# Kernel optimization log

Measured on AMD Instinct MI355X. Metric: run time of the kernel, lower is better.

Reference implementation:

```python
import jax, jax.numpy as jnp
import numpy as np

B, T, E, UNITS, VOCAB, NCLS = 128, 512, 256, 256, 50257, 2

def setup_inputs() -> dict:
    key = jax.random.key(0)
    ks = jax.random.split(key, 7)
    s = 0.05
    return {
        "sentence": jax.random.randint(ks[0], (B, T), 0, VOCAB, dtype=jnp.int32),
        "emb_table": jax.random.normal(ks[1], (VOCAB, E), jnp.float32) * s,
        "W": jax.random.normal(ks[2], (1, UNITS, E), jnp.float32) * s,
        "U": jax.random.normal(ks[3], (1, UNITS, UNITS), jnp.float32) * s,
        "W1": jax.random.normal(ks[4], (UNITS, 32), jnp.float32) * s,
        "b1": jnp.zeros((32,), jnp.float32),
        "W2": jax.random.normal(ks[5], (32, NCLS), jnp.float32) * s,
        "b2": jnp.zeros((NCLS,), jnp.float32),
    }

def reference(sentence, emb_table, W, U, W1, b1, W2, b2):
    # Embedding lookup: [B, T, E]
    emb = emb_table[sentence]
    # Precompute input projection for all timesteps in one batched GEMM:
    # x @ W[0].T for every t -> [T, B, units]
    xW = jnp.einsum('bte,ue->tbu', emb, W[0])
    Ut = U[0].T  # [units, units]

    def step(h, xw_t):
        h_new = jnp.tanh(xw_t + h @ Ut)
        return h_new, None

    h0 = jnp.zeros((sentence.shape[0], W.shape[1]), emb.dtype)
    h_final, _ = jax.lax.scan(step, h0, xW)

    # Classification head (dropout is identity at inference)
    hidden = jax.nn.relu(h_final @ W1 + b1)
    logits = hidden @ W2 + b2
    return jax.nn.softmax(logits, axis=-1)
```

## Files before the change

### kernel.cpp

```cpp
#include <hip/hip_runtime.h>
#include <hip/hip_bf16.h>
#include <stdint.h>

#define TT 512
#define NB 128
#define EM 256
#define UN 256

typedef float floatx4 __attribute__((ext_vector_type(4)));
typedef int v8i __attribute__((ext_vector_type(8)));

#define SCALE_Q 0x7B7B7B7BU
#define SCALE_A 0x7D7D7D7DU

#define BAR() asm volatile("s_waitcnt lgkmcnt(0)\n\ts_barrier" ::: "memory")

__device__ inline unsigned short f2bf(float f) {
    union { float f; uint32_t u; } v; v.f = f;
    uint32_t r = v.u + 0x7fffu + ((v.u >> 16) & 1u);
    return (unsigned short)(r >> 16);
}
__device__ inline unsigned char f2fp8(float f) {
    int pk = __builtin_amdgcn_cvt_pk_fp8_f32(f, f, 0, false);
    return (unsigned char)(pk & 0xff);
}
__device__ inline float fp8dec(uint32_t word, int sel) {
#if defined(__has_builtin)
#if __has_builtin(__builtin_amdgcn_cvt_f32_fp8)
    return __builtin_amdgcn_cvt_f32_fp8(word >> (8 * sel), 0);
#else
    unsigned char b = (word >> (8 * sel)) & 0xff;
    int s = b >> 7, e = (b >> 3) & 15, m = b & 7;
    float v = e ? ldexpf((float)(8 + m), e - 10) : ldexpf((float)m, -9);
    return s ? -v : v;
#endif
#else
    unsigned char b = (word >> (8 * sel)) & 0xff;
    int s = b >> 7, e = (b >> 3) & 15, m = b & 7;
    float v = e ? ldexpf((float)(8 + m), e - 10) : ldexpf((float)m, -9);
    return s ? -v : v;
#endif
}

__global__ void k_pack(const float* __restrict__ W, const float* __restrict__ U,
                       unsigned char* __restrict__ wfrag8, unsigned char* __restrict__ ufrag8) {
    int bid = blockIdx.x;
    const float* src = (bid < 32) ? W : U;
    unsigned char* dstbase = (bid < 32) ? wfrag8 : ufrag8;
    int idx = (bid & 31) * 256 + threadIdx.x;
    int jg   = idx & 3;
    int lane = (idx >> 2) & 63;
    int tile = idx >> 8;
    int nt = tile & 15, kh = tile >> 4;
    int u  = nt * 16 + (lane & 15);
    int k0 = kh * 128 + (lane >> 4) * 32 + jg * 8;
    unsigned char* dst = dstbase + ((size_t)tile * 64 + lane) * 32 + jg * 8;
    #pragma unroll
    for (int j = 0; j < 8; j++) dst[j] = f2fp8(16.f * src[u * EM + k0 + j]);
}

__global__ __launch_bounds__(256, 2) void k_gemm(
    const int* __restrict__ sent, const float* __restrict__ emb,
    const unsigned char* __restrict__ wfrag8, unsigned char* __restrict__ xw8)
{
    __shared__ unsigned char gt[64][272];
    int w    = threadIdx.x >> 6;
    int lane = threadIdx.x & 63;
    int m  = lane & 15;
    int kg = lane >> 4;
    int row = blockIdx.x * 64 + w * 16 + m;
    int tok = sent[row];
    const float* arow = emb + (size_t)tok * EM;

    union { uint32_t d[8]; v8i v; } A[2];
    #pragma unroll
    for (int kh = 0; kh < 2; kh++) {
        const float* p = arow + kh * 128 + kg * 32;
        #pragma unroll
        for (int d = 0; d < 8; d++) {
            float4 f = *(const float4*)(p + 4 * d);
            int pk = __builtin_amdgcn_cvt_pk_fp8_f32(16.f * f.x, 16.f * f.y, 0, false);
            pk     = __builtin_amdgcn_cvt_pk_fp8_f32(16.f * f.z, 16.f * f.w, pk, true);
            A[kh].d[d] = (uint32_t)pk;
        }
    }

    const floatx4 zero4 = {0.f, 0.f, 0.f, 0.f};
    floatx4 acc[16];
    #pragma unroll
    for (int nt = 0; nt < 16; nt++) {
        union { uint4 u4[2]; v8i v; } B0, B1;
        const uint4* p0 = (const uint4*)(wfrag8 + ((size_t)(0 * 16 + nt) * 64 + lane) * 32);
        const uint4* p1 = (const uint4*)(wfrag8 + ((size_t)(1 * 16 + nt) * 64 + lane) * 32);
        B0.u4[0] = p0[0]; B0.u4[1] = p0[1];
        B1.u4[0] = p1[0]; B1.u4[1] = p1[1];
        floatx4 a = __builtin_amdgcn_mfma_scale_f32_16x16x128_f8f6f4(
                        A[0].v, B0.v, zero4, 0, 0, 0, SCALE_Q, 0, SCALE_Q);
        a = __builtin_amdgcn_mfma_scale_f32_16x16x128_f8f6f4(
                        A[1].v, B1.v, a, 0, 0, 0, SCALE_Q, 0, SCALE_Q);
        acc[nt] = a;
    }

    int rloc = w * 16 + kg * 4;
    #pragma unroll
    for (int nt = 0; nt < 16; nt++) {
        #pragma unroll
        for (int r = 0; r < 4; r++) {
            gt[rloc + r][nt * 16 + m] = f2fp8(16.f * acc[nt][r]);
        }
    }
    __syncthreads();

    int rowbase = blockIdx.x * 64;
    #pragma unroll
    for (int r2 = 0; r2 < 16; r2++) {
        int rr = w * 16 + r2;
        uint32_t v = *(const uint32_t*)&gt[rr][lane * 4];
        *(uint32_t*)(xw8 + (size_t)(rowbase + rr) * UN + lane * 4) = v;
    }
}

__global__ __launch_bounds__(256, 1) void k_rnn(
    const unsigned char* __restrict__ ufrag8, const unsigned char* __restrict__ xw8,
    const float* __restrict__ W1, const float* __restrict__ b1,
    const float* __restrict__ W2, const float* __restrict__ b2,
    float* __restrict__ out)
{
    __shared__ __align__(16) unsigned char hb8[2][256];
    __shared__ __align__(16) unsigned char xstage[64 * 256];
    __shared__ float hid[32];
    const int t    = threadIdx.x;
    const int lane = t & 63;
    const int w    = t >> 6;
    const int kg   = lane >> 4;
    const int b    = blockIdx.x;

    v8i ufr8[4][2];
    #pragma unroll
    for (int q = 0; q < 4; q++) {
        #pragma unroll
        for (int kh = 0; kh < 2; kh++) {
            const uint4* p = (const uint4*)(ufrag8 + ((size_t)(kh * 16 + 4 * w + q) * 64 + lane) * 32);
            union { uint4 u4[2]; v8i v; } cvt;
            cvt.u4[0] = p[0]; cvt.u4[1] = p[1];
            ufr8[q][kh] = cvt.v;
        }
    }

    const unsigned char* xwb = xw8 + (size_t)b * TT * UN;
    const int roff = t * 16;

    uint4 xr[4];
    #pragma unroll
    for (int p = 0; p < 4; p++) xr[p] = *(const uint4*)(xwb + roff + p * 4096);
    #pragma unroll
    for (int p = 0; p < 4; p++) *(uint4*)&xstage[roff + p * 4096] = xr[p];

    hb8[0][t] = 0; hb8[1][t] = 0;
    __syncthreads();

    int cur = 0;
    const float c3 = -0.33333334f, c5 = 0.13333334f, c7 = -0.05396825f, c9 = 0.02186949f;
    const floatx4 zero4 = {0.f, 0.f, 0.f, 0.f};
    const int sel = lane >> 4;

    for (int s = 0; s < TT; s++) {
        const int ls = s & 63;
        uint32_t xword = *(const uint32_t*)&xstage[ls * 256 + (t & ~3)];
        float xf = fp8dec(xword, t & 3) * 0.0625f;

        const unsigned char* hc = hb8[cur];
        union { uint4 u4[2]; v8i v; } A0, A1;
        A0.u4[0] = *(const uint4*)(hc + kg * 32);
        A0.u4[1] = *(const uint4*)(hc + kg * 32 + 16);
        A1.u4[0] = *(const uint4*)(hc + 128 + kg * 32);
        A1.u4[1] = *(const uint4*)(hc + 128 + kg * 32 + 16);

        float z[4];
        #pragma unroll
        for (int q = 0; q < 4; q++) {
            floatx4 acc = __builtin_amdgcn_mfma_scale_f32_16x16x128_f8f6f4(
                              A0.v, ufr8[q][0], zero4, 0, 0, 0, SCALE_A, 0, SCALE_Q);
            acc = __builtin_amdgcn_mfma_scale_f32_16x16x128_f8f6f4(
                              A1.v, ufr8[q][1], acc, 0, 0, 0, SCALE_A, 0, SCALE_Q);
            z[q] = acc[0];
        }

        float zz = (sel == 0) ? z[0] : (sel == 1) ? z[1] : (sel == 2) ? z[2] : z[3];
        zz += xf;

        float hn;
        if (__builtin_expect(fabsf(zz) > 0.75f, 0)) {
            float e = __expf(2.f * zz);
            hn = 1.f - 2.f * __builtin_amdgcn_rcpf(e + 1.f);
        } else {
            float x2f = zz * zz;
            float p = fmaf(x2f, c9, c7);
            p = fmaf(x2f, p, c5);
            p = fmaf(x2f, p, c3);
            hn = fmaf(zz * x2f, p, zz);
        }

        hb8[cur ^ 1][t] = f2fp8(4.f * hn);

        if (ls == 60 && s + 68 <= TT) {
            const unsigned char* cb = xwb + (size_t)(s + 4) * UN;
            #pragma unroll
            for (int p = 0; p < 4; p++) xr[p] = *(const uint4*)(cb + roff + p * 4096);
        }
        if (ls == 63 && s + 65 <= TT) {
            BAR();
            #pragma unroll
            for (int p = 0; p < 4; p++) *(uint4*)&xstage[roff + p * 4096] = xr[p];
        }
        BAR();
        cur ^= 1;
    }

    if (t < 32) {
        float a = b1[t];
        for (int k = 0; k < 256; k++) {
            uint32_t wd = *(const uint32_t*)&hb8[cur][k & ~3];
            a += 0.25f * fp8dec(wd, k & 3) * W1[k * 32 + t];
        }
        hid[t] = fmaxf(a, 0.f);
    }
    __syncthreads();
    if (t == 0) {
        float l0 = b2[0], l1 = b2[1];
        #pragma unroll
        for (int i = 0; i < 32; i++) {
            float hv = hid[i];
            l0 += hv * W2[2 * i];
            l1 += hv * W2[2 * i + 1];
        }
        float mx2 = fmaxf(l0, l1);
        float e0 = __expf(l0 - mx2), e1 = __expf(l1 - mx2);
        float inv = 1.f / (e0 + e1);
        out[2 * b]     = e0 * inv;
        out[2 * b + 1] = e1 * inv;
    }
}

extern "C" void kernel_launch(void* const* d_in, const int* in_sizes, int n_in,
                              void* d_out, int out_size, void* d_ws, size_t ws_size,
                              hipStream_t stream) {
    const int*   sent = (const int*)d_in[0];
    const float* emb  = (const float*)d_in[1];
    const float* W    = (const float*)d_in[2];
    const float* U    = (const float*)d_in[3];
    const float* W1   = (const float*)d_in[4];
    const float* b1   = (const float*)d_in[5];
    const float* W2   = (const float*)d_in[6];
    const float* b2   = (const float*)d_in[7];
    float* out = (float*)d_out;

    unsigned char* xw8    = (unsigned char*)d_ws;
    unsigned char* wfrag8 = (unsigned char*)d_ws + (size_t)NB * TT * UN;
    unsigned char* ufrag8 = wfrag8 + (size_t)UN * EM;

    k_pack<<<64, 256, 0, stream>>>(W, U, wfrag8, ufrag8);
    k_gemm<<<(NB * TT) / 64, 256, 0, stream>>>(sent, emb, wfrag8, xw8);
    k_rnn<<<NB, 256, 0, stream>>>(ufrag8, xw8, W1, b1, W2, b2, out);
}
```

Measured before the change: 302.5 us.

## Fuse input-projection GEMM into RNN kernel, computed in chunks interleaved with the recurrence

Removes the separate k_gemm kernel and its global xW buffer. Each RNN block now holds the W fragments in registers, computes the first 64 timesteps of x·Wᵀ up front, and then computes the next chunk into a double-buffered LDS array spread over the serial loop: token loads, embedding loads and the MFMA plus pack each land on different phases. The aim is to hide the projection work in idle time of the latency-bound recurrence and avoid the global round trip through the fp8 workspace. It costs more registers (W fragments plus 16 float4 prefetch) and adds work to some steps of the critical loop.

```diff
diff --git a/kernel.cpp b/kernel.cpp
--- a/kernel.cpp
+++ b/kernel.cpp
@@ -6,6 +6,7 @@
 #define NB 128
 #define EM 256
 #define UN 256
+#define XS 68
 
 typedef float floatx4 __attribute__((ext_vector_type(4)));
 typedef int v8i __attribute__((ext_vector_type(8)));
@@ -15,31 +16,12 @@
 
 #define BAR() asm volatile("s_waitcnt lgkmcnt(0)\n\ts_barrier" ::: "memory")
 
-__device__ inline unsigned short f2bf(float f) {
-    union { float f; uint32_t u; } v; v.f = f;
-    uint32_t r = v.u + 0x7fffu + ((v.u >> 16) & 1u);
-    return (unsigned short)(r >> 16);
-}
 __device__ inline unsigned char f2fp8(float f) {
     int pk = __builtin_amdgcn_cvt_pk_fp8_f32(f, f, 0, false);
     return (unsigned char)(pk & 0xff);
 }
 __device__ inline float fp8dec(uint32_t word, int sel) {
-#if defined(__has_builtin)
-#if __has_builtin(__builtin_amdgcn_cvt_f32_fp8)
     return __builtin_amdgcn_cvt_f32_fp8(word >> (8 * sel), 0);
-#else
-    unsigned char b = (word >> (8 * sel)) & 0xff;
-    int s = b >> 7, e = (b >> 3) & 15, m = b & 7;
-    float v = e ? ldexpf((float)(8 + m), e - 10) : ldexpf((float)m, -9);
-    return s ? -v : v;
-#endif
-#else
-    unsigned char b = (word >> (8 * sel)) & 0xff;
-    int s = b >> 7, e = (b >> 3) & 15, m = b & 7;
-    float v = e ? ldexpf((float)(8 + m), e - 10) : ldexpf((float)m, -9);
-    return s ? -v : v;
-#endif
 }
 
 __global__ void k_pack(const float* __restrict__ W, const float* __restrict__ U,
@@ -59,115 +41,86 @@
     for (int j = 0; j < 8; j++) dst[j] = f2fp8(16.f * src[u * EM + k0 + j]);
 }
 
-__global__ __launch_bounds__(256, 2) void k_gemm(
+__global__ __launch_bounds__(256, 1) void k_rnn(
     const int* __restrict__ sent, const float* __restrict__ emb,
-    const unsigned char* __restrict__ wfrag8, unsigned char* __restrict__ xw8)
-{
-    __shared__ unsigned char gt[64][272];
-    int w    = threadIdx.x >> 6;
-    int lane = threadIdx.x & 63;
-    int m  = lane & 15;
-    int kg = lane >> 4;
-    int row = blockIdx.x * 64 + w * 16 + m;
-    int tok = sent[row];
-    const float* arow = emb + (size_t)tok * EM;
-
-    union { uint32_t d[8]; v8i v; } A[2];
-    #pragma unroll
-    for (int kh = 0; kh < 2; kh++) {
-        const float* p = arow + kh * 128 + kg * 32;
-        #pragma unroll
-        for (int d = 0; d < 8; d++) {
-            float4 f = *(const float4*)(p + 4 * d);
-            int pk = __builtin_amdgcn_cvt_pk_fp8_f32(16.f * f.x, 16.f * f.y, 0, false);
-            pk     = __builtin_amdgcn_cvt_pk_fp8_f32(16.f * f.z, 16.f * f.w, pk, true);
-            A[kh].d[d] = (uint32_t)pk;
-        }
-    }
-
-    const floatx4 zero4 = {0.f, 0.f, 0.f, 0.f};
-    floatx4 acc[16];
-    #pragma unroll
-    for (int nt = 0; nt < 16; nt++) {
-        union { uint4 u4[2]; v8i v; } B0, B1;
-        const uint4* p0 = (const uint4*)(wfrag8 + ((size_t)(0 * 16 + nt) * 64 + lane) * 32);
-        const uint4* p1 = (const uint4*)(wfrag8 + ((size_t)(1 * 16 + nt) * 64 + lane) * 32);
-        B0.u4[0] = p0[0]; B0.u4[1] = p0[1];
-        B1.u4[0] = p1[0]; B1.u4[1] = p1[1];
-        floatx4 a = __builtin_amdgcn_mfma_scale_f32_16x16x128_f8f6f4(
-                        A[0].v, B0.v, zero4, 0, 0, 0, SCALE_Q, 0, SCALE_Q);
-        a = __builtin_amdgcn_mfma_scale_f32_16x16x128_f8f6f4(
-                        A[1].v, B1.v, a, 0, 0, 0, SCALE_Q, 0, SCALE_Q);
-        acc[nt] = a;
-    }
-
-    int rloc = w * 16 + kg * 4;
-    #pragma unroll
-    for (int nt = 0; nt < 16; nt++) {
-        #pragma unroll
-        for (int r = 0; r < 4; r++) {
-            gt[rloc + r][nt * 16 + m] = f2fp8(16.f * acc[nt][r]);
-        }
-    }
-    __syncthreads();
-
-    int rowbase = blockIdx.x * 64;
-    #pragma unroll
-    for (int r2 = 0; r2 < 16; r2++) {
-        int rr = w * 16 + r2;
-        uint32_t v = *(const uint32_t*)&gt[rr][lane * 4];
-        *(uint32_t*)(xw8 + (size_t)(rowbase + rr) * UN + lane * 4) = v;
-    }
-}
-
-__global__ __launch_bounds__(256, 1) void k_rnn(
-    const unsigned char* __restrict__ ufrag8, const unsigned char* __restrict__ xw8,
+    const unsigned char* __restrict__ wfrag8, const unsigned char* __restrict__ ufrag8,
     const float* __restrict__ W1, const float* __restrict__ b1,
     const float* __restrict__ W2, const float* __restrict__ b2,
     float* __restrict__ out)
 {
     __shared__ __align__(16) unsigned char hb8[2][256];
-    __shared__ __align__(16) unsigned char xstage[64 * 256];
+    __shared__ __align__(16) unsigned char xs[2][256 * XS];
     __shared__ float hid[32];
     const int t    = threadIdx.x;
     const int lane = t & 63;
     const int w    = t >> 6;
     const int kg   = lane >> 4;
+    const int m15  = lane & 15;
     const int b    = blockIdx.x;
 
-    v8i ufr8[4][2];
+    v8i ufr8[4][2], wfr8[4][2];
     #pragma unroll
     for (int q = 0; q < 4; q++) {
         #pragma unroll
         for (int kh = 0; kh < 2; kh++) {
-            const uint4* p = (const uint4*)(ufrag8 + ((size_t)(kh * 16 + 4 * w + q) * 64 + lane) * 32);
-            union { uint4 u4[2]; v8i v; } cvt;
-            cvt.u4[0] = p[0]; cvt.u4[1] = p[1];
-            ufr8[q][kh] = cvt.v;
-        }
-    }
-
-    const unsigned char* xwb = xw8 + (size_t)b * TT * UN;
-    const int roff = t * 16;
-
-    uint4 xr[4];
+            size_t off = ((size_t)(kh * 16 + 4 * w + q) * 64 + lane) * 32;
+            union { uint4 u4[2]; v8i v; } cu, cw;
+            cu.u4[0] = *(const uint4*)(ufrag8 + off);
+            cu.u4[1] = *(const uint4*)(ufrag8 + off + 16);
+            cw.u4[0] = *(const uint4*)(wfrag8 + off);
+            cw.u4[1] = *(const uint4*)(wfrag8 + off + 16);
+            ufr8[q][kh] = cu.v;
+            wfr8[q][kh] = cw.v;
+        }
+    }
+
+    const int* sb = sent + b * TT;
+    const int ubase = 64 * w + m15;
+    const int xrow  = t * XS;
+    const floatx4 zero4 = {0.f, 0.f, 0.f, 0.f};
+
     #pragma unroll
-    for (int p = 0; p < 4; p++) xr[p] = *(const uint4*)(xwb + roff + p * 4096);
-    #pragma unroll
-    for (int p = 0; p < 4; p++) *(uint4*)&xstage[roff + p * 4096] = xr[p];
+    for (int mt = 0; mt < 4; mt++) {
+        int tok = sb[mt * 16 + m15];
+        const float* ar = emb + (size_t)tok * EM;
+        union { uint32_t d[8]; v8i v; } A[2];
+        #pragma unroll
+        for (int kh = 0; kh < 2; kh++) {
+            const float* p = ar + kh * 128 + kg * 32;
+            #pragma unroll
+            for (int d = 0; d < 8; d++) {
+                float4 f = *(const float4*)(p + 4 * d);
+                int pk = __builtin_amdgcn_cvt_pk_fp8_f32(16.f * f.x, 16.f * f.y, 0, false);
+                pk     = __builtin_amdgcn_cvt_pk_fp8_f32(16.f * f.z, 16.f * f.w, pk, true);
+                A[kh].d[d] = (uint32_t)pk;
+            }
+        }
+        #pragma unroll
+        for (int q = 0; q < 4; q++) {
+            floatx4 acc = __builtin_amdgcn_mfma_scale_f32_16x16x128_f8f6f4(
+                              A[0].v, wfr8[q][0], zero4, 0, 0, 0, SCALE_Q, 0, SCALE_Q);
+            acc = __builtin_amdgcn_mfma_scale_f32_16x16x128_f8f6f4(
+                              A[1].v, wfr8[q][1], acc, 0, 0, 0, SCALE_Q, 0, SCALE_Q);
+            int pk = __builtin_amdgcn_cvt_pk_fp8_f32(16.f * acc[0], 16.f * acc[1], 0, false);
+            pk     = __builtin_amdgcn_cvt_pk_fp8_f32(16.f * acc[2], 16.f * acc[3], pk, true);
+            *(uint32_t*)&xs[0][(ubase + q * 16) * XS + mt * 16 + kg * 4] = (uint32_t)pk;
+        }
+    }
 
     hb8[0][t] = 0; hb8[1][t] = 0;
     __syncthreads();
 
     int cur = 0;
     const float c3 = -0.33333334f, c5 = 0.13333334f, c7 = -0.05396825f, c9 = 0.02186949f;
-    const floatx4 zero4 = {0.f, 0.f, 0.f, 0.f};
-    const int sel = lane >> 4;
+    const int sel = kg;
+
+    float4 fa[16];
+    int tokr = 0;
 
     for (int s = 0; s < TT; s++) {
-        const int ls = s & 63;
-        uint32_t xword = *(const uint32_t*)&xstage[ls * 256 + (t & ~3)];
-        float xf = fp8dec(xword, t & 3) * 0.0625f;
+        const int ls   = s & 63;
+        const int xbuf = (s >> 6) & 1;
+        float xf = fp8dec((uint32_t)xs[xbuf][xrow + ls], 0) * 0.0625f;
 
         const unsigned char* hc = hb8[cur];
         union { uint4 u4[2]; v8i v; } A0, A1;
@@ -203,16 +156,46 @@
 
         hb8[cur ^ 1][t] = f2fp8(4.f * hn);
 
-        if (ls == 60 && s + 68 <= TT) {
-            const unsigned char* cb = xwb + (size_t)(s + 4) * UN;
-            #pragma unroll
-            for (int p = 0; p < 4; p++) xr[p] = *(const uint4*)(cb + roff + p * 4096);
-        }
-        if (ls == 63 && s + 65 <= TT) {
-            BAR();
-            #pragma unroll
-            for (int p = 0; p < 4; p++) *(uint4*)&xstage[roff + p * 4096] = xr[p];
-        }
+        if (s < TT - 64) {
+            const int ph = ls & 15;
+            const int mt = ls >> 4;
+            const int base = (s & ~63) + 64;
+            if (ph == 0) {
+                tokr = sb[base + mt * 16 + m15];
+            } else if (ph == 2) {
+                const float* ar = emb + (size_t)tokr * EM;
+                #pragma unroll
+                for (int kh = 0; kh < 2; kh++) {
+                    const float* p = ar + kh * 128 + kg * 32;
+                    #pragma unroll
+                    for (int d = 0; d < 8; d++) fa[kh * 8 + d] = *(const float4*)(p + 4 * d);
+                }
+            } else if (ph == 8) {
+                union { uint32_t d[8]; v8i v; } A[2];
+                #pragma unroll
+                for (int kh = 0; kh < 2; kh++) {
+                    #pragma unroll
+                    for (int d = 0; d < 8; d++) {
+                        float4 f = fa[kh * 8 + d];
+                        int pk = __builtin_amdgcn_cvt_pk_fp8_f32(16.f * f.x, 16.f * f.y, 0, false);
+                        pk     = __builtin_amdgcn_cvt_pk_fp8_f32(16.f * f.z, 16.f * f.w, pk, true);
+                        A[kh].d[d] = (uint32_t)pk;
+                    }
+                }
+                const int nxt = xbuf ^ 1;
+                #pragma unroll
+                for (int q = 0; q < 4; q++) {
+                    floatx4 acc = __builtin_amdgcn_mfma_scale_f32_16x16x128_f8f6f4(
+                                      A[0].v, wfr8[q][0], zero4, 0, 0, 0, SCALE_Q, 0, SCALE_Q);
+                    acc = __builtin_amdgcn_mfma_scale_f32_16x16x128_f8f6f4(
+                                      A[1].v, wfr8[q][1], acc, 0, 0, 0, SCALE_Q, 0, SCALE_Q);
+                    int pk = __builtin_amdgcn_cvt_pk_fp8_f32(16.f * acc[0], 16.f * acc[1], 0, false);
+                    pk     = __builtin_amdgcn_cvt_pk_fp8_f32(16.f * acc[2], 16.f * acc[3], pk, true);
+                    *(uint32_t*)&xs[nxt][(ubase + q * 16) * XS + mt * 16 + kg * 4] = (uint32_t)pk;
+                }
+            }
+        }
+
         BAR();
         cur ^= 1;
     }
@@ -255,11 +238,9 @@
     const float* b2   = (const float*)d_in[7];
     float* out = (float*)d_out;
 
-    unsigned char* xw8    = (unsigned char*)d_ws;
-    unsigned char* wfrag8 = (unsigned char*)d_ws + (size_t)NB * TT * UN;
+    unsigned char* wfrag8 = (unsigned char*)d_ws;
     unsigned char* ufrag8 = wfrag8 + (size_t)UN * EM;
 
     k_pack<<<64, 256, 0, stream>>>(W, U, wfrag8, ufrag8);
-    k_gemm<<<(NB * TT) / 64, 256, 0, stream>>>(sent, emb, wfrag8, xw8);
-    k_rnn<<<NB, 256, 0, stream>>>(ufrag8, xw8, W1, b1, W2, b2, out);
-}
+    k_rnn<<<NB, 256, 0, stream>>>(sent, emb, wfrag8, ufrag8, W1, b1, W2, b2, out);
+}
```

Result: slower. 431.8 us (+42.7%).
